# Kernel tuning notes

Measured on AMD Instinct MI355X. Metric: run time of the kernel, lower is better.

The kernel has to match this reference:

```python
import jax, jax.numpy as jnp
import numpy as np

# e2m1 FP4 value table: sign bit in nibble MSB, values {0,0.5,1,1.5,2,3,4,6}
_E2M1 = jnp.array([0.0, 0.5, 1.0, 1.5, 2.0, 3.0, 4.0, 6.0,
                   -0.0, -0.5, -1.0, -1.5, -2.0, -3.0, -4.0, -6.0], dtype=jnp.float32)


def _dequant_fp4(packed, scales, group_size):
    """packed: [E, out, in//8] uint32; scales: [E, in//group_size, out] -> [E, out, in] f32."""
    shifts = jnp.arange(8, dtype=jnp.uint32) * 4  # nibble shift amounts 0,4,...,28
    nib = (packed[..., None] >> shifts) & jnp.uint32(0xF)  # [E, out, in//8, 8]
    E, O, P, _ = nib.shape
    nib = nib.reshape(E, O, P * 8).astype(jnp.int32)
    w = _E2M1[nib]  # [E, out, in] f32
    gids = jnp.arange(P * 8) // group_size  # group id per input column
    sc = jnp.transpose(scales, (0, 2, 1))[:, :, gids]  # [E, out, in]
    return w * sc


def setup_inputs() -> dict:
    E, H, I, T, K, G = 8, 2048, 1408, 2048, 2, 128
    key = jax.random.key(0)
    ks = jax.random.split(key, 9)
    x = jax.random.normal(ks[0], (T, H), dtype=jnp.float32)
    gate_packed = jax.random.bits(ks[1], (E, I, H // 8), dtype=jnp.uint32)
    up_packed = jax.random.bits(ks[2], (E, I, H // 8), dtype=jnp.uint32)
    down_packed = jax.random.bits(ks[3], (E, H, I // 8), dtype=jnp.uint32)
    gate_scales = jax.random.uniform(ks[4], (E, H // G, I), jnp.float32, 0.5, 1.5)
    up_scales = jax.random.uniform(ks[5], (E, H // G, I), jnp.float32, 0.5, 1.5)
    down_scales = jax.random.uniform(ks[6], (E, I // G, H), jnp.float32, 0.5, 1.5)
    topk_idx = jax.random.randint(ks[7], (T, K), 0, E, dtype=jnp.int32)
    w = jax.random.uniform(ks[8], (T, K), jnp.float32)
    topk_w = w / jnp.sum(w, axis=-1, keepdims=True)
    return {"x": x,
            "gate_packed": gate_packed, "gate_scales": gate_scales,
            "up_packed": up_packed, "up_scales": up_scales,
            "down_packed": down_packed, "down_scales": down_scales,
            "topk_idx": topk_idx, "topk_w": topk_w, "group_size": G}


def reference(x, gate_packed, gate_scales, up_packed, up_scales,
              down_packed, down_scales, topk_idx, topk_w, group_size):
    # Fused dequant (nibble unpack + e2m1 table + per-group scale) for all experts
    gate_w = _dequant_fp4(gate_packed, gate_scales, group_size)  # [E, I, H]
    up_w = _dequant_fp4(up_packed, up_scales, group_size)        # [E, I, H]
    down_w = _dequant_fp4(down_packed, down_scales, group_size)  # [E, H, I]
    # Grouped SwiGLU expert MLP (dense over E=8 experts, gather routed outputs)
    g = jnp.einsum('th,eih->eti', x, gate_w)
    u = jnp.einsum('th,eih->eti', x, up_w)
    h = jax.nn.silu(g) * u                                        # [E, T, I]
    y = jnp.einsum('eti,ehi->eth', h, down_w)                     # [E, T, H]
    T = x.shape[0]
    sel = y[topk_idx, jnp.arange(T)[:, None], :]                  # [T, K, H]
    return jnp.sum(sel * topk_w[..., None], axis=1)               # [T, H]
```

## Files before the change

### kernel.cpp

```cpp
#include <hip/hip_runtime.h>
#include <hip/hip_bf16.h>
#include <stdint.h>

#define E_ 8
#define H_ 2048
#define I_ 1408
#define T_ 2048
#define K_ 2
#define G_ 128

typedef __bf16 bf16;
typedef bf16 bf16x8 __attribute__((ext_vector_type(8)));
typedef float f32x4 __attribute__((ext_vector_type(4)));

__device__ __forceinline__ uint32_t prm(uint32_t hi, uint32_t lo, uint32_t sel) {
    return __builtin_amdgcn_perm(hi, lo, sel);
}

struct DequantTab { uint32_t thi0, thi1, tlo0, tlo1; };

__device__ __forceinline__ DequantTab build_tab(float s) {
    union { bf16 h[8]; uint32_t u[4]; } tb;
    tb.h[0] = (bf16)(0.0f);
    tb.h[1] = (bf16)(0.5f * s);
    tb.h[2] = (bf16)(1.0f * s);
    tb.h[3] = (bf16)(1.5f * s);
    tb.h[4] = (bf16)(2.0f * s);
    tb.h[5] = (bf16)(3.0f * s);
    tb.h[6] = (bf16)(4.0f * s);
    tb.h[7] = (bf16)(6.0f * s);
    DequantTab t;
    t.thi0 = prm(tb.u[1], tb.u[0], 0x07050301u);
    t.tlo0 = prm(tb.u[1], tb.u[0], 0x06040200u);
    t.thi1 = prm(tb.u[3], tb.u[2], 0x07050301u);
    t.tlo1 = prm(tb.u[3], tb.u[2], 0x06040200u);
    return t;
}

__device__ __forceinline__ uint4 dequant8t(uint32_t p, const DequantTab& t) {
    const uint32_t pr = p >> 4;
    const uint32_t pe = p  & 0x07070707u;
    const uint32_t po = pr & 0x07070707u;
    const uint32_t He = prm(t.thi1, t.thi0, pe) | ((p  & 0x08080808u) << 4);
    const uint32_t Le = prm(t.tlo1, t.tlo0, pe);
    const uint32_t Ho = prm(t.thi1, t.thi0, po) | ((pr & 0x08080808u) << 4);
    const uint32_t Lo = prm(t.tlo1, t.tlo0, po);
    const uint32_t E01 = prm(He, Le, 0x05010400u);
    const uint32_t E23 = prm(He, Le, 0x07030602u);
    const uint32_t O01 = prm(Ho, Lo, 0x05010400u);
    const uint32_t O23 = prm(Ho, Lo, 0x07030602u);
    return make_uint4(prm(O01, E01, 0x05040100u),
                      prm(O01, E01, 0x07060302u),
                      prm(O23, E23, 0x05040100u),
                      prm(O23, E23, 0x07060302u));
}

__device__ __forceinline__ void gld16(void* lds, const void* g) {
    __builtin_amdgcn_global_load_lds(
        (__attribute__((address_space(1))) void*)g,
        (__attribute__((address_space(3))) void*)lds, 16, 0, 0);
}

__global__ void route_count(const int* __restrict__ topk_idx, int* __restrict__ counts) {
    int p = blockIdx.x * blockDim.x + threadIdx.x;
    if (p < T_ * K_) atomicAdd(&counts[topk_idx[p]], 1);
}

__global__ void route_scan(const int* __restrict__ counts, int* __restrict__ offsets,
                           int* __restrict__ tmap) {
    if (threadIdx.x == 0) {
        int acc = 0, ti = 0;
        for (int e = 0; e < E_; e++) {
            offsets[e] = acc;
            int nt = (counts[e] + 127) >> 7;
            for (int j = 0; j < nt; j++) tmap[ti++] = (e << 16) | j;
            acc += counts[e];
        }
        offsets[E_] = acc;
        for (; ti < 64; ti++) tmap[ti] = -1;
    }
}

__global__ void route_fill(const int* __restrict__ topk_idx, const float* __restrict__ topk_w,
                           int* __restrict__ cursors, const int* __restrict__ offsets,
                           int* __restrict__ tok, float* __restrict__ wgt,
                           int* __restrict__ inv) {
    int p = blockIdx.x * blockDim.x + threadIdx.x;
    if (p < T_ * K_) {
        int e = topk_idx[p];
        int slot = atomicAdd(&cursors[e], 1);
        int idx = offsets[e] + slot;
        tok[idx] = p / K_;
        wgt[idx] = topk_w[p];
        inv[p] = idx;
    }
}

__global__ __launch_bounds__(256)
void xcast_kernel(const float* __restrict__ x, uint4* __restrict__ xb) {
    const int i = blockIdx.x * 256 + threadIdx.x;
    const float4 a = ((const float4*)x)[i * 2];
    const float4 b = ((const float4*)x)[i * 2 + 1];
    union { uint4 u; bf16 h[8]; } r;
    r.h[0] = (bf16)a.x; r.h[1] = (bf16)a.y; r.h[2] = (bf16)a.z; r.h[3] = (bf16)a.w;
    r.h[4] = (bf16)b.x; r.h[5] = (bf16)b.y; r.h[6] = (bf16)b.z; r.h[7] = (bf16)b.w;
    xb[i] = r.u;
}

__global__ __launch_bounds__(256, 3)
void gemm1t_kernel(const bf16* __restrict__ xb,
                   const uint32_t* __restrict__ gate_packed,
                   const float* __restrict__ gate_scales,
                   const uint32_t* __restrict__ up_packed,
                   const float* __restrict__ up_scales,
                   const int* __restrict__ offsets,
                   const int* __restrict__ tmap,
                   const int* __restrict__ tok, bf16* __restrict__ h_buf)
{
    const int tm = tmap[blockIdx.x];
    if (tm < 0) return;
    const int e = tm >> 16, ty = tm & 0xffff;
    const int row0 = offsets[e];
    const int cnt = offsets[e + 1] - row0;
    const int itile = blockIdx.y;

    __shared__ __align__(16) bf16 xs[2][128][64];
    __shared__ __align__(16) bf16 wgs[64][64];
    __shared__ __align__(16) bf16 wus[64][64];

    const int tid = threadIdx.x;

    const int xr = tid >> 3;
    const int xc = tid & 7;
    const int xch = (xc ^ (xr & 7)) * 8;
    const bf16* xsrc[4];
    bf16* xdst[4];
#pragma unroll
    for (int j = 0; j < 4; ++j) {
        int g = ty * 128 + xr + j * 32;
        g = (g < cnt) ? g : (cnt - 1);
        xsrc[j] = xb + (size_t)tok[row0 + g] * H_ + xch;
        xdst[j] = &xs[0][xr + j * 32][xc * 8];
    }

    const int mat  = tid >> 7;
    const int id   = tid & 127;
    const int wrow = id >> 1;
    const int quad = id & 1;
    const int irow = itile * 64 + wrow;
    const uint32_t* wp_row = (mat ? up_packed : gate_packed)
        + (size_t)e * I_ * (H_ / 8) + (size_t)irow * (H_ / 8) + quad * 4;
    const float* ws_row = (mat ? up_scales : gate_scales)
        + (size_t)e * (H_ / G_) * I_ + irow;
    bf16 (* const wdst)[64] = mat ? wus : wgs;

    const int wave = tid >> 6, lane = tid & 63;
    const int wy = wave >> 1, wx = wave & 1;
    const int lrow = lane & 15, kq = lane >> 4;

    f32x4 accg[4][2] = {};
    f32x4 accu[4][2] = {};

    float sc_cur = ws_row[0];
    uint4 pw = *(const uint4*)(wp_row);
#pragma unroll
    for (int j = 0; j < 4; ++j) gld16(xdst[j], xsrc[j]);

    constexpr int NG = H_ / G_;
    constexpr int NT = 2 * NG;
    for (int kg = 0; kg < NG; ++kg) {
        const int kgn = (kg + 1 < NG) ? kg + 1 : kg;
        const float sc_nxt = ws_row[(size_t)kgn * I_];
        const DequantTab tw = build_tab(sc_cur);
#pragma unroll
        for (int kh2 = 0; kh2 < 2; ++kh2) {
            const int t  = kg * 2 + kh2;
            const int tn = (t < NT - 1) ? t + 1 : t;
            const uint4 pwn = *(const uint4*)(wp_row + tn * 8);
#pragma unroll
            for (int j = 0; j < 4; ++j)
                gld16(xdst[j] + (kh2 ^ 1) * (128 * 64), xsrc[j] + tn * 64);
            __builtin_amdgcn_sched_barrier(0);
            {
                uint4 d0 = dequant8t(pw.x, tw);
                uint4 d1 = dequant8t(pw.y, tw);
                uint4 d2 = dequant8t(pw.z, tw);
                uint4 d3 = dequant8t(pw.w, tw);
                const int cb = quad * 4, rs = wrow & 7;
                *(uint4*)&wdst[wrow][((cb + 0) ^ rs) * 8] = d0;
                *(uint4*)&wdst[wrow][((cb + 1) ^ rs) * 8] = d1;
                *(uint4*)&wdst[wrow][((cb + 2) ^ rs) * 8] = d2;
                *(uint4*)&wdst[wrow][((cb + 3) ^ rs) * 8] = d3;
            }
            __builtin_amdgcn_sched_barrier(0);
            if (kh2 == 0) asm volatile("s_waitcnt vmcnt(6) lgkmcnt(0)" ::: "memory");
            else          asm volatile("s_waitcnt vmcnt(5) lgkmcnt(0)" ::: "memory");
            __builtin_amdgcn_s_barrier();
            __builtin_amdgcn_sched_barrier(0);
#pragma unroll
            for (int kh = 0; kh < 2; ++kh) {
                bf16x8 a[4], bg[2], bu[2];
#pragma unroll
                for (int mi = 0; mi < 4; ++mi) {
                    const int ra = wy * 64 + mi * 16 + lrow;
                    a[mi] = *(const bf16x8*)&xs[kh2][ra][((kh * 4 + kq) ^ (ra & 7)) * 8];
                }
#pragma unroll
                for (int ni = 0; ni < 2; ++ni) {
                    const int rb = wx * 32 + ni * 16 + lrow;
                    const int cb2 = ((kh * 4 + kq) ^ (rb & 7)) * 8;
                    bg[ni] = *(const bf16x8*)&wgs[rb][cb2];
                    bu[ni] = *(const bf16x8*)&wus[rb][cb2];
                }
#pragma unroll
                for (int mi = 0; mi < 4; ++mi)
#pragma unroll
                    for (int ni = 0; ni < 2; ++ni) {
                        accg[mi][ni] = __builtin_amdgcn_mfma_f32_16x16x32_bf16(a[mi], bg[ni], accg[mi][ni], 0, 0, 0);
                        accu[mi][ni] = __builtin_amdgcn_mfma_f32_16x16x32_bf16(a[mi], bu[ni], accu[mi][ni], 0, 0, 0);
                    }
            }
            __builtin_amdgcn_sched_barrier(0);
            asm volatile("s_waitcnt lgkmcnt(0)" ::: "memory");
            __builtin_amdgcn_s_barrier();
            pw = pwn;
        }
        sc_cur = sc_nxt;
    }

#pragma unroll
    for (int mi = 0; mi < 4; ++mi)
#pragma unroll
        for (int ni = 0; ni < 2; ++ni) {
            const int icol = itile * 64 + wx * 32 + ni * 16 + lrow;
#pragma unroll
            for (int r = 0; r < 4; ++r) {
                const int grow = ty * 128 + wy * 64 + mi * 16 + kq * 4 + r;
                if (grow < cnt) {
                    const float gv = accg[mi][ni][r];
                    const float hv = gv / (1.f + __expf(-gv)) * accu[mi][ni][r];
                    h_buf[(size_t)(row0 + grow) * I_ + icol] = (bf16)hv;
                }
            }
        }
}

__global__ __launch_bounds__(256, 3)
void gemm2t_kernel(const bf16* __restrict__ h_buf,
                   const uint32_t* __restrict__ down_packed,
                   const float* __restrict__ down_scales,
                   const int* __restrict__ offsets,
                   const int* __restrict__ tmap,
                   const float* __restrict__ wgt, float* __restrict__ yp)
{
    const int tm = tmap[blockIdx.x];
    if (tm < 0) return;
    const int e = tm >> 16, ty = tm & 0xffff;
    const int row0 = offsets[e];
    const int cnt = offsets[e + 1] - row0;
    const int htile = blockIdx.y;

    __shared__ __align__(16) bf16 hs[2][128][64];
    __shared__ __align__(16) bf16 wds[128][64];

    const int tid = threadIdx.x;

    const int xr = tid >> 3;
    const int xc = tid & 7;
    const int xch = (xc ^ (xr & 7)) * 8;
    const bf16* hsrc[4];
    bf16* hdst[4];
#pragma unroll
    for (int j = 0; j < 4; ++j) {
        int g = ty * 128 + xr + j * 32;
        g = (g < cnt) ? g : (cnt - 1);
        hsrc[j] = h_buf + (size_t)(row0 + g) * I_ + xch;
        hdst[j] = &hs[0][xr + j * 32][xc * 8];
    }

    const int wrow = tid >> 1;
    const int quad = tid & 1;
    const int hrow = htile * 128 + wrow;
    const uint32_t* dp_row = down_packed + (size_t)e * H_ * (I_ / 8) + (size_t)hrow * (I_ / 8) + quad * 4;
    const float* ds_row = down_scales + (size_t)e * (I_ / G_) * H_ + hrow;

    const int wave = tid >> 6, lane = tid & 63;
    const int wy = wave >> 1, wx = wave & 1;
    const int lrow = lane & 15, kq = lane >> 4;

    f32x4 acc[4][4] = {};

    float sc_cur = ds_row[0];
    uint4 pw = *(const uint4*)(dp_row);
#pragma unroll
    for (int j = 0; j < 4; ++j) gld16(hdst[j], hsrc[j]);

    constexpr int NG = I_ / G_;
    constexpr int NT = 2 * NG;
    for (int kg = 0; kg < NG; ++kg) {
        const int kgn = (kg + 1 < NG) ? kg + 1 : kg;
        const float sc_nxt = ds_row[(size_t)kgn * H_];
        const DequantTab td = build_tab(sc_cur);
#pragma unroll
        for (int kh2 = 0; kh2 < 2; ++kh2) {
            const int t  = kg * 2 + kh2;
            const int tn = (t < NT - 1) ? t + 1 : t;
            const uint4 pwn = *(const uint4*)(dp_row + tn * 8);
#pragma unroll
            for (int j = 0; j < 4; ++j)
                gld16(hdst[j] + (kh2 ^ 1) * (128 * 64), hsrc[j] + tn * 64);
            __builtin_amdgcn_sched_barrier(0);
            {
                uint4 d0 = dequant8t(pw.x, td);
                uint4 d1 = dequant8t(pw.y, td);
                uint4 d2 = dequant8t(pw.z, td);
                uint4 d3 = dequant8t(pw.w, td);
                const int cb = quad * 4, rs = wrow & 7;
                *(uint4*)&wds[wrow][((cb + 0) ^ rs) * 8] = d0;
                *(uint4*)&wds[wrow][((cb + 1) ^ rs) * 8] = d1;
                *(uint4*)&wds[wrow][((cb + 2) ^ rs) * 8] = d2;
                *(uint4*)&wds[wrow][((cb + 3) ^ rs) * 8] = d3;
            }
            __builtin_amdgcn_sched_barrier(0);
            if (kh2 == 0) asm volatile("s_waitcnt vmcnt(6) lgkmcnt(0)" ::: "memory");
            else          asm volatile("s_waitcnt vmcnt(5) lgkmcnt(0)" ::: "memory");
            __builtin_amdgcn_s_barrier();
            __builtin_amdgcn_sched_barrier(0);
#pragma unroll
            for (int kh = 0; kh < 2; ++kh) {
                bf16x8 a[4], b[4];
#pragma unroll
                for (int mi = 0; mi < 4; ++mi) {
                    const int ra = wy * 64 + mi * 16 + lrow;
                    a[mi] = *(const bf16x8*)&hs[kh2][ra][((kh * 4 + kq) ^ (ra & 7)) * 8];
                }
#pragma unroll
                for (int ni = 0; ni < 4; ++ni) {
                    const int rb = wx * 64 + ni * 16 + lrow;
                    b[ni] = *(const bf16x8*)&wds[rb][((kh * 4 + kq) ^ (rb & 7)) * 8];
                }
#pragma unroll
                for (int mi = 0; mi < 4; ++mi)
#pragma unroll
                    for (int ni = 0; ni < 4; ++ni)
                        acc[mi][ni] = __builtin_amdgcn_mfma_f32_16x16x32_bf16(a[mi], b[ni], acc[mi][ni], 0, 0, 0);
            }
            __builtin_amdgcn_sched_barrier(0);
            asm volatile("s_waitcnt lgkmcnt(0)" ::: "memory");
            __builtin_amdgcn_s_barrier();
            pw = pwn;
        }
        sc_cur = sc_nxt;
    }

#pragma unroll
    for (int mi = 0; mi < 4; ++mi)
#pragma unroll
        for (int r = 0; r < 4; ++r) {
            const int grow = ty * 128 + wy * 64 + mi * 16 + kq * 4 + r;
            if (grow < cnt) {
                const float w = wgt[row0 + grow];
#pragma unroll
                for (int ni = 0; ni < 4; ++ni) {
                    const int col = htile * 128 + wx * 64 + ni * 16 + lrow;
                    yp[(size_t)(row0 + grow) * H_ + col] = acc[mi][ni][r] * w;
                }
            }
        }
}

__global__ __launch_bounds__(256)
void combine_kernel(const float* __restrict__ yp, const int* __restrict__ inv,
                    float* __restrict__ out) {
    const int idx = blockIdx.x * 256 + threadIdx.x;
    const int t = idx >> 9;
    const int c = idx & 511;
    const float4 a = ((const float4*)yp)[(size_t)inv[t * 2] * (H_ / 4) + c];
    const float4 b = ((const float4*)yp)[(size_t)inv[t * 2 + 1] * (H_ / 4) + c];
    float4 o;
    o.x = a.x + b.x; o.y = a.y + b.y; o.z = a.z + b.z; o.w = a.w + b.w;
    ((float4*)out)[idx] = o;
}

extern "C" void kernel_launch(void* const* d_in, const int* in_sizes, int n_in,
                              void* d_out, int out_size, void* d_ws, size_t ws_size,
                              hipStream_t stream) {
    const float* x = (const float*)d_in[0];
    const uint32_t* gate_packed = (const uint32_t*)d_in[1];
    const float* gate_scales = (const float*)d_in[2];
    const uint32_t* up_packed = (const uint32_t*)d_in[3];
    const float* up_scales = (const float*)d_in[4];
    const uint32_t* down_packed = (const uint32_t*)d_in[5];
    const float* down_scales = (const float*)d_in[6];
    const int* topk_idx = (const int*)d_in[7];
    const float* topk_w = (const float*)d_in[8];
    float* out = (float*)d_out;

    char* ws = (char*)d_ws;
    int* counts  = (int*)ws;
    int* cursors = (int*)(ws + 32);
    int* offsets = (int*)(ws + 64);
    int* tmap    = (int*)(ws + 128);
    int* tok     = (int*)(ws + 640);
    float* wgt   = (float*)(ws + 17024);
    int* inv     = (int*)(ws + 33408);
    bf16* h_buf  = (bf16*)(ws + 49792);
    bf16* xb     = (bf16*)(ws + 49792 + 11534336ull);
    float* yp    = (float*)(ws + 49792 + 11534336ull + 8388608ull);

    hipMemsetAsync(d_ws, 0, 1024, stream);

    route_count<<<(T_ * K_ + 255) / 256, 256, 0, stream>>>(topk_idx, counts);
    route_scan<<<1, 64, 0, stream>>>(counts, offsets, tmap);
    route_fill<<<(T_ * K_ + 255) / 256, 256, 0, stream>>>(topk_idx, topk_w, cursors, offsets,
                                                          tok, wgt, inv);
    xcast_kernel<<<T_ * H_ / 8 / 256, 256, 0, stream>>>(x, (uint4*)xb);

    dim3 g1(40, I_ / 64);
    gemm1t_kernel<<<g1, 256, 0, stream>>>(xb, gate_packed, gate_scales, up_packed, up_scales,
                                          offsets, tmap, tok, h_buf);
    dim3 g2(40, H_ / 128);
    gemm2t_kernel<<<g2, 256, 0, stream>>>(h_buf, down_packed, down_scales,
                                          offsets, tmap, wgt, yp);
    combine_kernel<<<T_ * H_ / 4 / 256, 256, 0, stream>>>(yp, inv, out);
}
```

Measured before the change: 271.6 us.

## Enlarge GEMM blocks to 512 threads and map each expert's blocks to one XCD

Both grouped GEMMs now run 512-thread blocks with larger weight tiles: 128 intermediate rows in gemm1 and 256 hidden rows in gemm2. Each dequantized weight tile is therefore reused across more MFMA work. The routing table now gives each expert five fixed slots, and the last slot loops over any leftover 128-token chunks. Block ids are interleaved so that bid&7 selects the expert, which is meant to keep each expert's weights within one XCD's L2. The trade-offs are fewer, heavier blocks, possible load imbalance when an expert has more than five chunks, and changed occupancy and register pressure.

```diff
diff --git a/kernel.cpp b/kernel.cpp
--- a/kernel.cpp
+++ b/kernel.cpp
@@ -69,15 +69,15 @@
 __global__ void route_scan(const int* __restrict__ counts, int* __restrict__ offsets,
                            int* __restrict__ tmap) {
     if (threadIdx.x == 0) {
-        int acc = 0, ti = 0;
+        int acc = 0;
+        for (int e = 0; e < E_; e++) { offsets[e] = acc; acc += counts[e]; }
+        offsets[E_] = acc;
+        for (int s = 0; s < 40; s++) tmap[s] = -1;
         for (int e = 0; e < E_; e++) {
-            offsets[e] = acc;
             int nt = (counts[e] + 127) >> 7;
-            for (int j = 0; j < nt; j++) tmap[ti++] = (e << 16) | j;
-            acc += counts[e];
+            if (nt > 5) nt = 5;
+            for (int j = 0; j < nt; j++) tmap[e * 5 + j] = (e << 16) | j;
         }
-        offsets[E_] = acc;
-        for (; ti < 64; ti++) tmap[ti] = -1;
     }
 }
 
@@ -107,7 +107,7 @@
     xb[i] = r.u;
 }
 
-__global__ __launch_bounds__(256, 3)
+__global__ __launch_bounds__(512, 4)
 void gemm1t_kernel(const bf16* __restrict__ xb,
                    const uint32_t* __restrict__ gate_packed,
                    const float* __restrict__ gate_scales,
@@ -117,37 +117,30 @@
                    const int* __restrict__ tmap,
                    const int* __restrict__ tok, bf16* __restrict__ h_buf)
 {
-    const int tm = tmap[blockIdx.x];
+    const int bid = blockIdx.x;
+    const int x8 = bid & 7;
+    const int r = bid >> 3;
+    const int t5 = r / 11;
+    const int itile = r - t5 * 11;
+    const int tm = tmap[x8 * 5 + t5];
     if (tm < 0) return;
-    const int e = tm >> 16, ty = tm & 0xffff;
+    const int e = tm >> 16, j0 = tm & 0xffff;
     const int row0 = offsets[e];
     const int cnt = offsets[e + 1] - row0;
-    const int itile = blockIdx.y;
+    const int nch = (cnt + 127) >> 7;
+    const int chend = (j0 == 4) ? nch : (j0 + 1);
 
     __shared__ __align__(16) bf16 xs[2][128][64];
-    __shared__ __align__(16) bf16 wgs[64][64];
-    __shared__ __align__(16) bf16 wus[64][64];
+    __shared__ __align__(16) bf16 wgs[128][64];
+    __shared__ __align__(16) bf16 wus[128][64];
 
     const int tid = threadIdx.x;
 
-    const int xr = tid >> 3;
-    const int xc = tid & 7;
-    const int xch = (xc ^ (xr & 7)) * 8;
-    const bf16* xsrc[4];
-    bf16* xdst[4];
-#pragma unroll
-    for (int j = 0; j < 4; ++j) {
-        int g = ty * 128 + xr + j * 32;
-        g = (g < cnt) ? g : (cnt - 1);
-        xsrc[j] = xb + (size_t)tok[row0 + g] * H_ + xch;
-        xdst[j] = &xs[0][xr + j * 32][xc * 8];
-    }
-
-    const int mat  = tid >> 7;
-    const int id   = tid & 127;
-    const int wrow = id >> 1;
-    const int quad = id & 1;
-    const int irow = itile * 64 + wrow;
+    const int wr_  = tid >> 1;
+    const int mat  = wr_ >> 7;
+    const int wrow = wr_ & 127;
+    const int quad = tid & 1;
+    const int irow = itile * 128 + wrow;
     const uint32_t* wp_row = (mat ? up_packed : gate_packed)
         + (size_t)e * I_ * (H_ / 8) + (size_t)irow * (H_ / 8) + quad * 4;
     const float* ws_row = (mat ? up_scales : gate_scales)
@@ -155,97 +148,121 @@
     bf16 (* const wdst)[64] = mat ? wus : wgs;
 
     const int wave = tid >> 6, lane = tid & 63;
-    const int wy = wave >> 1, wx = wave & 1;
+    const int wy = wave >> 2, wx = wave & 3;
     const int lrow = lane & 15, kq = lane >> 4;
 
-    f32x4 accg[4][2] = {};
-    f32x4 accu[4][2] = {};
-
-    float sc_cur = ws_row[0];
-    uint4 pw = *(const uint4*)(wp_row);
-#pragma unroll
-    for (int j = 0; j < 4; ++j) gld16(xdst[j], xsrc[j]);
+    const int xr = tid >> 3;
+    const int xc = tid & 7;
+    const int xch = (xc ^ (xr & 7)) * 8;
 
     constexpr int NG = H_ / G_;
     constexpr int NT = 2 * NG;
-    for (int kg = 0; kg < NG; ++kg) {
-        const int kgn = (kg + 1 < NG) ? kg + 1 : kg;
-        const float sc_nxt = ws_row[(size_t)kgn * I_];
-        const DequantTab tw = build_tab(sc_cur);
-#pragma unroll
-        for (int kh2 = 0; kh2 < 2; ++kh2) {
-            const int t  = kg * 2 + kh2;
-            const int tn = (t < NT - 1) ? t + 1 : t;
-            const uint4 pwn = *(const uint4*)(wp_row + tn * 8);
-#pragma unroll
-            for (int j = 0; j < 4; ++j)
-                gld16(xdst[j] + (kh2 ^ 1) * (128 * 64), xsrc[j] + tn * 64);
-            __builtin_amdgcn_sched_barrier(0);
-            {
-                uint4 d0 = dequant8t(pw.x, tw);
-                uint4 d1 = dequant8t(pw.y, tw);
-                uint4 d2 = dequant8t(pw.z, tw);
-                uint4 d3 = dequant8t(pw.w, tw);
-                const int cb = quad * 4, rs = wrow & 7;
-                *(uint4*)&wdst[wrow][((cb + 0) ^ rs) * 8] = d0;
-                *(uint4*)&wdst[wrow][((cb + 1) ^ rs) * 8] = d1;
-                *(uint4*)&wdst[wrow][((cb + 2) ^ rs) * 8] = d2;
-                *(uint4*)&wdst[wrow][((cb + 3) ^ rs) * 8] = d3;
+
+    for (int ch = j0; ch < chend; ++ch) {
+        const bf16 *xsrc0, *xsrc1;
+        {
+            int g0 = ch * 128 + xr;        g0 = (g0 < cnt) ? g0 : (cnt - 1);
+            int g1 = ch * 128 + xr + 64;   g1 = (g1 < cnt) ? g1 : (cnt - 1);
+            xsrc0 = xb + (size_t)tok[row0 + g0] * H_ + xch;
+            xsrc1 = xb + (size_t)tok[row0 + g1] * H_ + xch;
+        }
+        bf16* xdst0 = &xs[0][xr][xc * 8];
+        bf16* xdst1 = &xs[0][xr + 64][xc * 8];
+
+        f32x4 accg[4][2] = {};
+        f32x4 accu[4][2] = {};
+
+        gld16(xdst0, xsrc0);
+        gld16(xdst1, xsrc1);
+        __builtin_amdgcn_sched_barrier(0);
+        uint4 pw = *(const uint4*)wp_row;
+        float sc_cur = ws_row[0];
+
+        for (int kg = 0; kg < NG; ++kg) {
+            const DequantTab tw = build_tab(sc_cur);
+            float sc_nxt = sc_cur;
+#pragma unroll
+            for (int kh2 = 0; kh2 < 2; ++kh2) {
+                const int t = kg * 2 + kh2;
+                const int tn = (t < NT - 1) ? t + 1 : t;
+                if (t < NT - 1) {
+                    const int nb = (kh2 ^ 1) * (128 * 64);
+                    gld16(xdst0 + nb, xsrc0 + tn * 64);
+                    gld16(xdst1 + nb, xsrc1 + tn * 64);
+                }
+                __builtin_amdgcn_sched_barrier(0);
+                const uint4 pwn = *(const uint4*)(wp_row + tn * 8);
+                if (kh2 == 0) {
+                    const int kgn = (kg + 1 < NG) ? kg + 1 : kg;
+                    sc_nxt = ws_row[(size_t)kgn * I_];
+                }
+                __builtin_amdgcn_sched_barrier(0);
+                {
+                    uint4 d0 = dequant8t(pw.x, tw);
+                    uint4 d1 = dequant8t(pw.y, tw);
+                    uint4 d2 = dequant8t(pw.z, tw);
+                    uint4 d3 = dequant8t(pw.w, tw);
+                    const int cb = quad * 4, rs = wrow & 7;
+                    *(uint4*)&wdst[wrow][((cb + 0) ^ rs) * 8] = d0;
+                    *(uint4*)&wdst[wrow][((cb + 1) ^ rs) * 8] = d1;
+                    *(uint4*)&wdst[wrow][((cb + 2) ^ rs) * 8] = d2;
+                    *(uint4*)&wdst[wrow][((cb + 3) ^ rs) * 8] = d3;
+                }
+                __builtin_amdgcn_sched_barrier(0);
+                if (kh2 == 0) asm volatile("s_waitcnt vmcnt(4) lgkmcnt(0)" ::: "memory");
+                else          asm volatile("s_waitcnt vmcnt(3) lgkmcnt(0)" ::: "memory");
+                __builtin_amdgcn_s_barrier();
+                __builtin_amdgcn_sched_barrier(0);
+#pragma unroll
+                for (int kh = 0; kh < 2; ++kh) {
+                    bf16x8 a[4], bg[2], bu[2];
+#pragma unroll
+                    for (int mi = 0; mi < 4; ++mi) {
+                        const int ra = wy * 64 + mi * 16 + lrow;
+                        a[mi] = *(const bf16x8*)&xs[kh2][ra][((kh * 4 + kq) ^ (ra & 7)) * 8];
+                    }
+#pragma unroll
+                    for (int ni = 0; ni < 2; ++ni) {
+                        const int rb = wx * 32 + ni * 16 + lrow;
+                        const int cb2 = ((kh * 4 + kq) ^ (rb & 7)) * 8;
+                        bg[ni] = *(const bf16x8*)&wgs[rb][cb2];
+                        bu[ni] = *(const bf16x8*)&wus[rb][cb2];
+                    }
+#pragma unroll
+                    for (int mi = 0; mi < 4; ++mi)
+#pragma unroll
+                        for (int ni = 0; ni < 2; ++ni) {
+                            accg[mi][ni] = __builtin_amdgcn_mfma_f32_16x16x32_bf16(a[mi], bg[ni], accg[mi][ni], 0, 0, 0);
+                            accu[mi][ni] = __builtin_amdgcn_mfma_f32_16x16x32_bf16(a[mi], bu[ni], accu[mi][ni], 0, 0, 0);
+                        }
+                }
+                __builtin_amdgcn_sched_barrier(0);
+                asm volatile("s_waitcnt lgkmcnt(0)" ::: "memory");
+                __builtin_amdgcn_s_barrier();
+                pw = pwn;
             }
-            __builtin_amdgcn_sched_barrier(0);
-            if (kh2 == 0) asm volatile("s_waitcnt vmcnt(6) lgkmcnt(0)" ::: "memory");
-            else          asm volatile("s_waitcnt vmcnt(5) lgkmcnt(0)" ::: "memory");
-            __builtin_amdgcn_s_barrier();
-            __builtin_amdgcn_sched_barrier(0);
-#pragma unroll
-            for (int kh = 0; kh < 2; ++kh) {
-                bf16x8 a[4], bg[2], bu[2];
-#pragma unroll
-                for (int mi = 0; mi < 4; ++mi) {
-                    const int ra = wy * 64 + mi * 16 + lrow;
-                    a[mi] = *(const bf16x8*)&xs[kh2][ra][((kh * 4 + kq) ^ (ra & 7)) * 8];
-                }
-#pragma unroll
-                for (int ni = 0; ni < 2; ++ni) {
-                    const int rb = wx * 32 + ni * 16 + lrow;
-                    const int cb2 = ((kh * 4 + kq) ^ (rb & 7)) * 8;
-                    bg[ni] = *(const bf16x8*)&wgs[rb][cb2];
-                    bu[ni] = *(const bf16x8*)&wus[rb][cb2];
-                }
-#pragma unroll
-                for (int mi = 0; mi < 4; ++mi)
-#pragma unroll
-                    for (int ni = 0; ni < 2; ++ni) {
-                        accg[mi][ni] = __builtin_amdgcn_mfma_f32_16x16x32_bf16(a[mi], bg[ni], accg[mi][ni], 0, 0, 0);
-                        accu[mi][ni] = __builtin_amdgcn_mfma_f32_16x16x32_bf16(a[mi], bu[ni], accu[mi][ni], 0, 0, 0);
-                    }
+            sc_cur = sc_nxt;
+        }
+
+#pragma unroll
+        for (int mi = 0; mi < 4; ++mi)
+#pragma unroll
+            for (int ni = 0; ni < 2; ++ni) {
+                const int icol = itile * 128 + wx * 32 + ni * 16 + lrow;
+#pragma unroll
+                for (int rr = 0; rr < 4; ++rr) {
+                    const int grow = ch * 128 + wy * 64 + mi * 16 + kq * 4 + rr;
+                    if (grow < cnt) {
+                        const float gv = accg[mi][ni][rr];
+                        const float hv = gv / (1.f + __expf(-gv)) * accu[mi][ni][rr];
+                        h_buf[(size_t)(row0 + grow) * I_ + icol] = (bf16)hv;
+                    }
+                }
             }
-            __builtin_amdgcn_sched_barrier(0);
-            asm volatile("s_waitcnt lgkmcnt(0)" ::: "memory");
-            __builtin_amdgcn_s_barrier();
-            pw = pwn;
-        }
-        sc_cur = sc_nxt;
     }
-
-#pragma unroll
-    for (int mi = 0; mi < 4; ++mi)
-#pragma unroll
-        for (int ni = 0; ni < 2; ++ni) {
-            const int icol = itile * 64 + wx * 32 + ni * 16 + lrow;
-#pragma unroll
-            for (int r = 0; r < 4; ++r) {
-                const int grow = ty * 128 + wy * 64 + mi * 16 + kq * 4 + r;
-                if (grow < cnt) {
-                    const float gv = accg[mi][ni][r];
-                    const float hv = gv / (1.f + __expf(-gv)) * accu[mi][ni][r];
-                    h_buf[(size_t)(row0 + grow) * I_ + icol] = (bf16)hv;
-                }
-            }
-        }
-}
-
-__global__ __launch_bounds__(256, 3)
+}
+
+__global__ __launch_bounds__(512, 4)
 void gemm2t_kernel(const bf16* __restrict__ h_buf,
                    const uint32_t* __restrict__ down_packed,
                    const float* __restrict__ down_scales,
@@ -253,120 +270,137 @@
                    const int* __restrict__ tmap,
                    const float* __restrict__ wgt, float* __restrict__ yp)
 {
-    const int tm = tmap[blockIdx.x];
+    const int bid = blockIdx.x;
+    const int x8 = bid & 7;
+    const int r = bid >> 3;
+    const int t5 = r >> 3;
+    const int htile = r & 7;
+    const int tm = tmap[x8 * 5 + t5];
     if (tm < 0) return;
-    const int e = tm >> 16, ty = tm & 0xffff;
+    const int e = tm >> 16, j0 = tm & 0xffff;
     const int row0 = offsets[e];
     const int cnt = offsets[e + 1] - row0;
-    const int htile = blockIdx.y;
+    const int nch = (cnt + 127) >> 7;
+    const int chend = (j0 == 4) ? nch : (j0 + 1);
 
     __shared__ __align__(16) bf16 hs[2][128][64];
-    __shared__ __align__(16) bf16 wds[128][64];
+    __shared__ __align__(16) bf16 wds[256][64];
 
     const int tid = threadIdx.x;
+
+    const int wrow = tid >> 1;
+    const int quad = tid & 1;
+    const int hrow = htile * 256 + wrow;
+    const uint32_t* dp_row = down_packed + (size_t)e * H_ * (I_ / 8) + (size_t)hrow * (I_ / 8) + quad * 4;
+    const float* ds_row = down_scales + (size_t)e * (I_ / G_) * H_ + hrow;
+
+    const int wave = tid >> 6, lane = tid & 63;
+    const int wy = wave >> 2, wx = wave & 3;
+    const int lrow = lane & 15, kq = lane >> 4;
 
     const int xr = tid >> 3;
     const int xc = tid & 7;
     const int xch = (xc ^ (xr & 7)) * 8;
-    const bf16* hsrc[4];
-    bf16* hdst[4];
-#pragma unroll
-    for (int j = 0; j < 4; ++j) {
-        int g = ty * 128 + xr + j * 32;
-        g = (g < cnt) ? g : (cnt - 1);
-        hsrc[j] = h_buf + (size_t)(row0 + g) * I_ + xch;
-        hdst[j] = &hs[0][xr + j * 32][xc * 8];
-    }
-
-    const int wrow = tid >> 1;
-    const int quad = tid & 1;
-    const int hrow = htile * 128 + wrow;
-    const uint32_t* dp_row = down_packed + (size_t)e * H_ * (I_ / 8) + (size_t)hrow * (I_ / 8) + quad * 4;
-    const float* ds_row = down_scales + (size_t)e * (I_ / G_) * H_ + hrow;
-
-    const int wave = tid >> 6, lane = tid & 63;
-    const int wy = wave >> 1, wx = wave & 1;
-    const int lrow = lane & 15, kq = lane >> 4;
-
-    f32x4 acc[4][4] = {};
-
-    float sc_cur = ds_row[0];
-    uint4 pw = *(const uint4*)(dp_row);
-#pragma unroll
-    for (int j = 0; j < 4; ++j) gld16(hdst[j], hsrc[j]);
 
     constexpr int NG = I_ / G_;
     constexpr int NT = 2 * NG;
-    for (int kg = 0; kg < NG; ++kg) {
-        const int kgn = (kg + 1 < NG) ? kg + 1 : kg;
-        const float sc_nxt = ds_row[(size_t)kgn * H_];
-        const DequantTab td = build_tab(sc_cur);
-#pragma unroll
-        for (int kh2 = 0; kh2 < 2; ++kh2) {
-            const int t  = kg * 2 + kh2;
-            const int tn = (t < NT - 1) ? t + 1 : t;
-            const uint4 pwn = *(const uint4*)(dp_row + tn * 8);
-#pragma unroll
-            for (int j = 0; j < 4; ++j)
-                gld16(hdst[j] + (kh2 ^ 1) * (128 * 64), hsrc[j] + tn * 64);
-            __builtin_amdgcn_sched_barrier(0);
-            {
-                uint4 d0 = dequant8t(pw.x, td);
-                uint4 d1 = dequant8t(pw.y, td);
-                uint4 d2 = dequant8t(pw.z, td);
-                uint4 d3 = dequant8t(pw.w, td);
-                const int cb = quad * 4, rs = wrow & 7;
-                *(uint4*)&wds[wrow][((cb + 0) ^ rs) * 8] = d0;
-                *(uint4*)&wds[wrow][((cb + 1) ^ rs) * 8] = d1;
-                *(uint4*)&wds[wrow][((cb + 2) ^ rs) * 8] = d2;
-                *(uint4*)&wds[wrow][((cb + 3) ^ rs) * 8] = d3;
+
+    for (int ch = j0; ch < chend; ++ch) {
+        const bf16 *hsrc0, *hsrc1;
+        {
+            int g0 = ch * 128 + xr;        g0 = (g0 < cnt) ? g0 : (cnt - 1);
+            int g1 = ch * 128 + xr + 64;   g1 = (g1 < cnt) ? g1 : (cnt - 1);
+            hsrc0 = h_buf + (size_t)(row0 + g0) * I_ + xch;
+            hsrc1 = h_buf + (size_t)(row0 + g1) * I_ + xch;
+        }
+        bf16* hdst0 = &hs[0][xr][xc * 8];
+        bf16* hdst1 = &hs[0][xr + 64][xc * 8];
+
+        f32x4 acc[4][4] = {};
+
+        gld16(hdst0, hsrc0);
+        gld16(hdst1, hsrc1);
+        __builtin_amdgcn_sched_barrier(0);
+        uint4 pw = *(const uint4*)dp_row;
+        float sc_cur = ds_row[0];
+
+        for (int kg = 0; kg < NG; ++kg) {
+            const DequantTab td = build_tab(sc_cur);
+            float sc_nxt = sc_cur;
+#pragma unroll
+            for (int kh2 = 0; kh2 < 2; ++kh2) {
+                const int t = kg * 2 + kh2;
+                const int tn = (t < NT - 1) ? t + 1 : t;
+                if (t < NT - 1) {
+                    const int nb = (kh2 ^ 1) * (128 * 64);
+                    gld16(hdst0 + nb, hsrc0 + tn * 64);
+                    gld16(hdst1 + nb, hsrc1 + tn * 64);
+                }
+                __builtin_amdgcn_sched_barrier(0);
+                const uint4 pwn = *(const uint4*)(dp_row + tn * 8);
+                if (kh2 == 0) {
+                    const int kgn = (kg + 1 < NG) ? kg + 1 : kg;
+                    sc_nxt = ds_row[(size_t)kgn * H_];
+                }
+                __builtin_amdgcn_sched_barrier(0);
+                {
+                    uint4 d0 = dequant8t(pw.x, td);
+                    uint4 d1 = dequant8t(pw.y, td);
+                    uint4 d2 = dequant8t(pw.z, td);
+                    uint4 d3 = dequant8t(pw.w, td);
+                    const int cb = quad * 4, rs = wrow & 7;
+                    *(uint4*)&wds[wrow][((cb + 0) ^ rs) * 8] = d0;
+                    *(uint4*)&wds[wrow][((cb + 1) ^ rs) * 8] = d1;
+                    *(uint4*)&wds[wrow][((cb + 2) ^ rs) * 8] = d2;
+                    *(uint4*)&wds[wrow][((cb + 3) ^ rs) * 8] = d3;
+                }
+                __builtin_amdgcn_sched_barrier(0);
+                if (kh2 == 0) asm volatile("s_waitcnt vmcnt(4) lgkmcnt(0)" ::: "memory");
+                else          asm volatile("s_waitcnt vmcnt(3) lgkmcnt(0)" ::: "memory");
+                __builtin_amdgcn_s_barrier();
+                __builtin_amdgcn_sched_barrier(0);
+#pragma unroll
+                for (int kh = 0; kh < 2; ++kh) {
+                    bf16x8 a[4], b[4];
+#pragma unroll
+                    for (int mi = 0; mi < 4; ++mi) {
+                        const int ra = wy * 64 + mi * 16 + lrow;
+                        a[mi] = *(const bf16x8*)&hs[kh2][ra][((kh * 4 + kq) ^ (ra & 7)) * 8];
+                    }
+#pragma unroll
+                    for (int ni = 0; ni < 4; ++ni) {
+                        const int rb = wx * 64 + ni * 16 + lrow;
+                        b[ni] = *(const bf16x8*)&wds[rb][((kh * 4 + kq) ^ (rb & 7)) * 8];
+                    }
+#pragma unroll
+                    for (int mi = 0; mi < 4; ++mi)
+#pragma unroll
+                        for (int ni = 0; ni < 4; ++ni)
+                            acc[mi][ni] = __builtin_amdgcn_mfma_f32_16x16x32_bf16(a[mi], b[ni], acc[mi][ni], 0, 0, 0);
+                }
+                __builtin_amdgcn_sched_barrier(0);
+                asm volatile("s_waitcnt lgkmcnt(0)" ::: "memory");
+                __builtin_amdgcn_s_barrier();
+                pw = pwn;
             }
-            __builtin_amdgcn_sched_barrier(0);
-            if (kh2 == 0) asm volatile("s_waitcnt vmcnt(6) lgkmcnt(0)" ::: "memory");
-            else          asm volatile("s_waitcnt vmcnt(5) lgkmcnt(0)" ::: "memory");
-            __builtin_amdgcn_s_barrier();
-            __builtin_amdgcn_sched_barrier(0);
-#pragma unroll
-            for (int kh = 0; kh < 2; ++kh) {
-                bf16x8 a[4], b[4];
-#pragma unroll
-                for (int mi = 0; mi < 4; ++mi) {
-                    const int ra = wy * 64 + mi * 16 + lrow;
-                    a[mi] = *(const bf16x8*)&hs[kh2][ra][((kh * 4 + kq) ^ (ra & 7)) * 8];
-                }
-#pragma unroll
-                for (int ni = 0; ni < 4; ++ni) {
-                    const int rb = wx * 64 + ni * 16 + lrow;
-                    b[ni] = *(const bf16x8*)&wds[rb][((kh * 4 + kq) ^ (rb & 7)) * 8];
-                }
-#pragma unroll
-                for (int mi = 0; mi < 4; ++mi)
-#pragma unroll
-                    for (int ni = 0; ni < 4; ++ni)
-                        acc[mi][ni] = __builtin_amdgcn_mfma_f32_16x16x32_bf16(a[mi], b[ni], acc[mi][ni], 0, 0, 0);
+            sc_cur = sc_nxt;
+        }
+
+#pragma unroll
+        for (int mi = 0; mi < 4; ++mi)
+#pragma unroll
+            for (int rr = 0; rr < 4; ++rr) {
+                const int grow = ch * 128 + wy * 64 + mi * 16 + kq * 4 + rr;
+                if (grow < cnt) {
+                    const float w = wgt[row0 + grow];
+#pragma unroll
+                    for (int ni = 0; ni < 4; ++ni) {
+                        const int col = htile * 256 + wx * 64 + ni * 16 + lrow;
+                        yp[(size_t)(row0 + grow) * H_ + col] = acc[mi][ni][rr] * w;
+                    }
+                }
             }
-            __builtin_amdgcn_sched_barrier(0);
-            asm volatile("s_waitcnt lgkmcnt(0)" ::: "memory");
-            __builtin_amdgcn_s_barrier();
-            pw = pwn;
-        }
-        sc_cur = sc_nxt;
     }
-
-#pragma unroll
-    for (int mi = 0; mi < 4; ++mi)
-#pragma unroll
-        for (int r = 0; r < 4; ++r) {
-            const int grow = ty * 128 + wy * 64 + mi * 16 + kq * 4 + r;
-            if (grow < cnt) {
-                const float w = wgt[row0 + grow];
-#pragma unroll
-                for (int ni = 0; ni < 4; ++ni) {
-                    const int col = htile * 128 + wx * 64 + ni * 16 + lrow;
-                    yp[(size_t)(row0 + grow) * H_ + col] = acc[mi][ni][r] * w;
-                }
-            }
-        }
 }
 
 __global__ __launch_bounds__(256)
@@ -416,11 +450,10 @@
                                                           tok, wgt, inv);
     xcast_kernel<<<T_ * H_ / 8 / 256, 256, 0, stream>>>(x, (uint4*)xb);
 
-    dim3 g1(40, I_ / 64);
-    gemm1t_kernel<<<g1, 256, 0, stream>>>(xb, gate_packed, gate_scales, up_packed, up_scales,
-                                          offsets, tmap, tok, h_buf);
-    dim3 g2(40, H_ / 128);
-    gemm2t_kernel<<<g2, 256, 0, stream>>>(h_buf, down_packed, down_scales,
-                                          offsets, tmap, wgt, yp);
+    gemm1t_kernel<<<dim3(55 * 8), 512, 0, stream>>>(xb, gate_packed, gate_scales,
+                                                    up_packed, up_scales,
+                                                    offsets, tmap, tok, h_buf);
+    gemm2t_kernel<<<dim3(40 * 8), 512, 0, stream>>>(h_buf, down_packed, down_scales,
+                                                    offsets, tmap, wgt, yp);
     combine_kernel<<<T_ * H_ / 4 / 256, 256, 0, stream>>>(yp, inv, out);
 }
```

Result: slower. 306.5 us (+12.9%).
